# Kernel tuning notes

Measured on AMD Instinct MI355X. Metric: run time of the kernel, lower is better.

## Reference

```python
import jax, jax.numpy as jnp
import numpy as np

N_ATOMS = 100000
N_MOLS = 2500
MAX_NB = 10
HID = 256
ATOM_FDIM = 151
FEAT_DIM = 200
FFN_HID = 1024
N_TASKS = 12
LN_EPS = 1e-5


def setup_inputs() -> dict:
    key = jax.random.key(0)
    ks = jax.random.split(key, 12)
    atoms_per_mol = N_ATOMS // N_MOLS  # 40
    starts = jnp.arange(N_MOLS, dtype=jnp.int32) * atoms_per_mol
    sizes = jnp.full((N_MOLS,), atoms_per_mol, dtype=jnp.int32)
    a_scope = jnp.stack([starts, sizes], axis=1)  # [M, 2]
    d_in = HID + ATOM_FDIM  # 407
    d_ff = 4 * HID          # 1024
    d_mol_in = HID + FEAT_DIM  # 456
    def lin(k, fan_in, shape):
        return jax.random.uniform(k, shape, jnp.float32, -1.0, 1.0) / np.sqrt(fan_in)
    return {
        "atom_output": jax.random.normal(ks[0], (N_ATOMS, HID), jnp.float32),
        "original_f_atoms": jax.random.uniform(ks[1], (N_ATOMS, ATOM_FDIM), jnp.float32),
        "a2a": jax.random.randint(ks[2], (N_ATOMS, MAX_NB), 0, N_ATOMS, jnp.int32),
        "a_scope": a_scope,
        "features_batch": jax.random.normal(ks[3], (N_MOLS, FEAT_DIM), jnp.float32),
        "W1": lin(ks[4], d_in, (d_in, d_ff)), "b1": jnp.zeros((d_ff,), jnp.float32),
        "W2": lin(ks[5], d_ff, (d_ff, HID)), "b2": jnp.zeros((HID,), jnp.float32),
        "ln_g": jnp.ones((HID,), jnp.float32), "ln_b": jnp.zeros((HID,), jnp.float32),
        "Wm1": lin(ks[6], d_mol_in, (d_mol_in, FFN_HID)), "bm1": jnp.zeros((FFN_HID,), jnp.float32),
        "Wm2": lin(ks[7], FFN_HID, (FFN_HID, N_TASKS)), "bm2": jnp.zeros((N_TASKS,), jnp.float32),
    }


def reference(atom_output, original_f_atoms, a2a, a_scope, features_batch,
              W1, b1, W2, b2, ln_g, ln_b, Wm1, bm1, Wm2, bm2):
    # select_neighbor_and_aggregate: gather neighbor embeddings and sum
    aggr = atom_output[a2a].sum(axis=1)                      # [N, HID]
    x = jnp.concatenate([original_f_atoms, aggr], axis=1)    # [N, HID+ATOM_FDIM]
    # PositionwiseFeedForward (dropout = identity at eval)
    h = jax.nn.relu(x @ W1 + b1) @ W2 + b2                   # [N, HID]
    # SublayerConnection with x=None: LayerNorm (dropout identity)
    mu = h.mean(axis=-1, keepdims=True)
    var = ((h - mu) ** 2).mean(axis=-1, keepdims=True)
    h = (h - mu) * jax.lax.rsqrt(var + LN_EPS) * ln_g + ln_b
    # Readout: mean over variable-length a_scope ranges (segment mean)
    starts = a_scope[:, 0]
    sizes = a_scope[:, 1]
    n_mols = a_scope.shape[0]
    seg_ids = jnp.searchsorted(starts, jnp.arange(h.shape[0], dtype=starts.dtype), side="right") - 1
    sums = jax.ops.segment_sum(h, seg_ids, num_segments=n_mols)   # [M, HID]
    mol = sums / sizes[:, None].astype(h.dtype)
    # concat molecule-level features, then mol FFN (2 layers)
    mol = jnp.concatenate([mol, features_batch], axis=1)          # [M, HID+FEAT_DIM]
    out = jax.nn.relu(mol @ Wm1 + bm1) @ Wm2 + bm2                # [M, N_TASKS]
    return out
```

## Files before the change

### kernel.cpp

```cpp
#include <hip/hip_runtime.h>

typedef __attribute__((ext_vector_type(8))) short bfrag;
typedef __attribute__((ext_vector_type(4))) float f32x4;

__device__ __forceinline__ float bf2f(unsigned short u) {
    union { unsigned u32; float f; } cv; cv.u32 = ((unsigned)u) << 16; return cv.f;
}
__device__ __forceinline__ unsigned short f2bf(float f) {
    union { float f; unsigned u; } cv; cv.f = f;
    unsigned u = cv.u;
    unsigned r = (u + 0x7fffu + ((u >> 16) & 1u)) >> 16;
    return (unsigned short)r;
}
__device__ __forceinline__ void gll16(const void* g, void* l) {
    __builtin_amdgcn_global_load_lds(
        (const __attribute__((address_space(1))) unsigned int*)g,
        (__attribute__((address_space(3))) unsigned int*)l, 16, 0, 0);
}

__global__ void to_bf16(const float* __restrict__ src, unsigned short* __restrict__ dst, size_t n) {
    size_t i = ((size_t)blockIdx.x * 256 + threadIdx.x) * 8;
    if (i >= n) return;
    f32x4 a = __builtin_nontemporal_load(reinterpret_cast<const f32x4*>(src + i));
    f32x4 b = __builtin_nontemporal_load(reinterpret_cast<const f32x4*>(src + i + 4));
    ushort4 o0 = {f2bf(a.x), f2bf(a.y), f2bf(a.z), f2bf(a.w)};
    ushort4 o1 = {f2bf(b.x), f2bf(b.y), f2bf(b.z), f2bf(b.w)};
    *reinterpret_cast<ushort4*>(dst + i) = o0;
    *reinterpret_cast<ushort4*>(dst + i + 4) = o1;
}

__global__ void transpose_pad(const float* __restrict__ W, unsigned short* __restrict__ WT,
                              int R, int Cn, int Kp, int split, int shiftA, int split2, int shiftB) {
    __shared__ unsigned short tile[32][33];
    int r0 = blockIdx.x * 32, c0 = blockIdx.y * 32;
#pragma unroll
    for (int j = 0; j < 4; j++) {
        int r = r0 + threadIdx.y + j * 8;
        int c = c0 + threadIdx.x;
        float v = (r < R) ? W[(size_t)r * Cn + c] : 0.f;
        tile[threadIdx.y + j * 8][threadIdx.x] = f2bf(v);
    }
    __syncthreads();
#pragma unroll
    for (int j = 0; j < 4; j++) {
        int c = c0 + threadIdx.y + j * 8;
        int r = r0 + threadIdx.x;
        int kn = (r < split) ? r + shiftA : (r < split2 ? r + shiftB : r);
        WT[(size_t)c * Kp + kn] = tile[threadIdx.x][threadIdx.y + j * 8];
    }
}

__global__ __launch_bounds__(256) void gather2(const unsigned short* __restrict__ abf,
                                               const float* __restrict__ f_atoms,
                                               const int* __restrict__ a2a,
                                               unsigned short* __restrict__ xb, int n_real) {
    int r = blockIdx.x * 4 + (threadIdx.x >> 6);
    int lane = threadIdx.x & 63;
    unsigned short* xrow = xb + (size_t)r * 448;
    if (r >= n_real) {
        *reinterpret_cast<ushort4*>(xrow + lane * 4) = ushort4{0, 0, 0, 0};
        if (lane < 48) *reinterpret_cast<ushort4*>(xrow + 256 + lane * 4) = ushort4{0, 0, 0, 0};
        return;
    }
    int v = (lane < 10) ? a2a[(size_t)r * 10 + lane] : 0;
    ushort4 u[10];
#pragma unroll
    for (int j = 0; j < 10; j++) {
        int nbj = __shfl(v, j);
        u[j] = *reinterpret_cast<const ushort4*>(abf + (size_t)nbj * 256 + lane * 4);
    }
    float a0 = 0.f, a1 = 0.f, a2 = 0.f, a3 = 0.f;
#pragma unroll
    for (int j = 0; j < 10; j++) {
        a0 += bf2f(u[j].x);
        a1 += bf2f(u[j].y);
        a2 += bf2f(u[j].z);
        a3 += bf2f(u[j].w);
    }
    ushort4 o = {f2bf(a0), f2bf(a1), f2bf(a2), f2bf(a3)};
    *reinterpret_cast<ushort4*>(xrow + lane * 4) = o;
    const float* fr = f_atoms + (size_t)r * 151;
#pragma unroll
    for (int s = 0; s < 3; s++) {
        int c = lane + s * 64;
        if (c < 151) xrow[256 + c] = f2bf(__builtin_nontemporal_load(fr + c));
    }
    if (lane < 41) xrow[407 + lane] = 0;
}

template <int RELU>
__global__ __launch_bounds__(512, 2) void gemm256(const unsigned short* __restrict__ A,
                                                  const unsigned short* __restrict__ BT,
                                                  const float* __restrict__ bias,
                                                  unsigned short* __restrict__ C,
                                                  int NB, int N, int K) {
    __shared__ __align__(16) unsigned short As[256 * 64];
    __shared__ __align__(16) unsigned short Bs[128 * 64];
    const int t = threadIdx.x;
    const int lane = t & 63, wid = t >> 6;
    const int wm = wid >> 1, wn = wid & 1;
    const int la = lane & 15, hi = lane >> 4;

    const int nwg = gridDim.x, orig = blockIdx.x;
    const int q = nwg >> 3, r8 = nwg & 7;
    const int xcd = orig & 7, slot = orig >> 3;
    const int wgid = (xcd < r8 ? xcd * (q + 1) : r8 * (q + 1) + (xcd - r8) * q) + slot;
    const int bm = (wgid / NB) * 256, bn = (wgid % NB) * 128;

    f32x4 acc[4][4] = {};

    const int tr = t >> 3, ts = t & 7;
    const unsigned short* Ag = A + (size_t)(bm + tr) * K + (ts ^ (tr & 7)) * 8;
    const unsigned short* Bg = BT + (size_t)(bn + tr) * K + (ts ^ (tr & 7)) * 8;
    const int ldst = tr * 64 + ts * 8;

    for (int kt = 0; kt < K; kt += 64) {
        __builtin_amdgcn_s_barrier();
#pragma unroll
        for (int p = 0; p < 4; p++) gll16(Ag + (size_t)(p * 64) * K + kt, &As[p * 4096 + ldst]);
#pragma unroll
        for (int p = 0; p < 2; p++) gll16(Bg + (size_t)(p * 64) * K + kt, &Bs[p * 4096 + ldst]);
        asm volatile("s_waitcnt vmcnt(0)" ::: "memory");
        __builtin_amdgcn_s_barrier();
#pragma unroll
        for (int kk = 0; kk < 2; kk++) {
            bfrag a[4], b[4];
#pragma unroll
            for (int i = 0; i < 4; i++) {
                int row = wm * 64 + i * 16 + la;
                a[i] = *reinterpret_cast<const bfrag*>(&As[row * 64 + (((kk * 4 + hi) ^ (la & 7)) * 8)]);
            }
#pragma unroll
            for (int j = 0; j < 4; j++) {
                int row = wn * 64 + j * 16 + la;
                b[j] = *reinterpret_cast<const bfrag*>(&Bs[row * 64 + (((kk * 4 + hi) ^ (la & 7)) * 8)]);
            }
#pragma unroll
            for (int i = 0; i < 4; i++)
#pragma unroll
                for (int j = 0; j < 4; j++)
                    acc[i][j] = __builtin_amdgcn_mfma_f32_16x16x32_bf16(a[i], b[j], acc[i][j], 0, 0, 0);
        }
    }

#pragma unroll
    for (int j = 0; j < 4; j++) {
        int col = bn + wn * 64 + j * 16 + la;
        float bv = bias[col];
#pragma unroll
        for (int i = 0; i < 4; i++) {
            int rbase = bm + wm * 64 + i * 16 + hi * 4;
#pragma unroll
            for (int r = 0; r < 4; r++) {
                float v = acc[i][j][r] + bv;
                if (RELU) v = fmaxf(v, 0.f);
                C[(size_t)(rbase + r) * N + col] = f2bf(v);
            }
        }
    }
}

__global__ __launch_bounds__(512, 2) void gemm2k(const unsigned short* __restrict__ A,
                                                 const unsigned short* __restrict__ BT,
                                                 const float* __restrict__ bias,
                                                 unsigned short* __restrict__ C, int K) {
    __shared__ __align__(16) unsigned short As[128 * 64];
    __shared__ __align__(16) unsigned short Bs[256 * 64];
    const int t = threadIdx.x;
    const int lane = t & 63, wid = t >> 6;
    const int wm = wid >> 2, wn = wid & 3;
    const int la = lane & 15, hi = lane >> 4;
    const int N = 256;

    const int nwg = gridDim.x, orig = blockIdx.x;
    const int q = nwg >> 3, r8 = nwg & 7;
    const int xcd = orig & 7, slot = orig >> 3;
    const int wgid = (xcd < r8 ? xcd * (q + 1) : r8 * (q + 1) + (xcd - r8) * q) + slot;
    const int bm = wgid * 128;

    f32x4 acc[4][4] = {};

    const int tr = t >> 3, ts = t & 7;
    const unsigned short* Ag = A + (size_t)(bm + tr) * K + (ts ^ (tr & 7)) * 8;
    const unsigned short* Bg = BT + (size_t)tr * K + (ts ^ (tr & 7)) * 8;
    const int ldst = tr * 64 + ts * 8;

    for (int kt = 0; kt < K; kt += 64) {
        __builtin_amdgcn_s_barrier();
#pragma unroll
        for (int p = 0; p < 2; p++) gll16(Ag + (size_t)(p * 64) * K + kt, &As[p * 4096 + ldst]);
#pragma unroll
        for (int p = 0; p < 4; p++) gll16(Bg + (size_t)(p * 64) * K + kt, &Bs[p * 4096 + ldst]);
        asm volatile("s_waitcnt vmcnt(0)" ::: "memory");
        __builtin_amdgcn_s_barrier();
#pragma unroll
        for (int kk = 0; kk < 2; kk++) {
            bfrag a[4], b[4];
#pragma unroll
            for (int i = 0; i < 4; i++) {
                int row = wm * 64 + i * 16 + la;
                a[i] = *reinterpret_cast<const bfrag*>(&As[row * 64 + (((kk * 4 + hi) ^ (la & 7)) * 8)]);
            }
#pragma unroll
            for (int j = 0; j < 4; j++) {
                int row = wn * 64 + j * 16 + la;
                b[j] = *reinterpret_cast<const bfrag*>(&Bs[row * 64 + (((kk * 4 + hi) ^ (la & 7)) * 8)]);
            }
#pragma unroll
            for (int i = 0; i < 4; i++)
#pragma unroll
                for (int j = 0; j < 4; j++)
                    acc[i][j] = __builtin_amdgcn_mfma_f32_16x16x32_bf16(a[i], b[j], acc[i][j], 0, 0, 0);
        }
    }

#pragma unroll
    for (int j = 0; j < 4; j++) {
        int col = wn * 64 + j * 16 + la;
        float bv = bias[col];
#pragma unroll
        for (int i = 0; i < 4; i++) {
            int rbase = bm + wm * 64 + i * 16 + hi * 4;
#pragma unroll
            for (int r = 0; r < 4; r++)
                C[(size_t)(rbase + r) * N + col] = f2bf(acc[i][j][r] + bv);
        }
    }
}

__global__ __launch_bounds__(512) void seg_ln_mean(const unsigned short* __restrict__ h,
                                                   const int* __restrict__ a_scope,
                                                   const float* __restrict__ g,
                                                   const float* __restrict__ b,
                                                   const float* __restrict__ feats,
                                                   unsigned short* __restrict__ mol, int n_mols) {
    __shared__ float part[8][256];
    int m = blockIdx.x, t = threadIdx.x;
    unsigned short* mrow = mol + (size_t)m * 512;
    if (m >= n_mols) {
        mrow[t] = 0;
        return;
    }
    int w = t >> 6, lane = t & 63;
    int start = a_scope[2 * m], size = a_scope[2 * m + 1];
    float4 gv = *reinterpret_cast<const float4*>(g + lane * 4);
    float4 bv = *reinterpret_cast<const float4*>(b + lane * 4);
    float a0 = 0.f, a1 = 0.f, a2 = 0.f, a3 = 0.f;
    for (int r = w; r < size; r += 8) {
        const unsigned short* hp = h + (size_t)(start + r) * 256 + lane * 4;
        ushort4 u = *reinterpret_cast<const ushort4*>(hp);
        float v0 = bf2f(u.x), v1 = bf2f(u.y), v2 = bf2f(u.z), v3 = bf2f(u.w);
        float s = v0 + v1 + v2 + v3;
        float q2 = v0 * v0 + v1 * v1 + v2 * v2 + v3 * v3;
#pragma unroll
        for (int off = 32; off; off >>= 1) {
            s += __shfl_xor(s, off);
            q2 += __shfl_xor(q2, off);
        }
        float mean = s * (1.f / 256.f);
        float var = q2 * (1.f / 256.f) - mean * mean;
        float rs = rsqrtf(var + 1e-5f);
        a0 += (v0 - mean) * rs * gv.x + bv.x;
        a1 += (v1 - mean) * rs * gv.y + bv.y;
        a2 += (v2 - mean) * rs * gv.z + bv.z;
        a3 += (v3 - mean) * rs * gv.w + bv.w;
    }
    part[w][lane * 4 + 0] = a0;
    part[w][lane * 4 + 1] = a1;
    part[w][lane * 4 + 2] = a2;
    part[w][lane * 4 + 3] = a3;
    __syncthreads();
    if (t < 256) {
        float sum = 0.f;
#pragma unroll
        for (int i = 0; i < 8; i++) sum += part[i][t];
        mrow[t] = f2bf(sum / (float)size);
    } else {
        int c = t - 256;
        float fv = (c < 200) ? feats[(size_t)m * 200 + c] : 0.f;
        mrow[256 + c] = f2bf(fv);
    }
}

__global__ void ffn2(const unsigned short* __restrict__ m1, const float* __restrict__ Wm2,
                     const float* __restrict__ bm2, float* __restrict__ out, int n_mols) {
    int wid = blockIdx.x * 4 + (threadIdx.x >> 6);
    if (wid >= n_mols) return;
    int lane = threadIdx.x & 63;
    float acc[12] = {};
    const unsigned short* row = m1 + (size_t)wid * 1024;
#pragma unroll 4
    for (int i = 0; i < 16; i++) {
        int k = i * 64 + lane;
        float v = bf2f(row[k]);
        const float* wr_ = Wm2 + (size_t)k * 12;
#pragma unroll
        for (int tsk = 0; tsk < 12; tsk++) acc[tsk] += v * wr_[tsk];
    }
#pragma unroll
    for (int tsk = 0; tsk < 12; tsk++) {
        float sv = acc[tsk];
#pragma unroll
        for (int off = 32; off; off >>= 1) sv += __shfl_xor(sv, off);
        if (lane == 0) out[(size_t)wid * 12 + tsk] = sv + bm2[tsk];
    }
}

extern "C" void kernel_launch(void* const* d_in, const int* in_sizes, int n_in,
                              void* d_out, int out_size, void* d_ws, size_t ws_size,
                              hipStream_t stream) {
    const float* atom_output = (const float*)d_in[0];
    const float* f_atoms     = (const float*)d_in[1];
    const int*   a2a         = (const int*)d_in[2];
    const int*   a_scope     = (const int*)d_in[3];
    const float* feats       = (const float*)d_in[4];
    const float* W1  = (const float*)d_in[5];
    const float* b1  = (const float*)d_in[6];
    const float* W2  = (const float*)d_in[7];
    const float* b2  = (const float*)d_in[8];
    const float* ln_g = (const float*)d_in[9];
    const float* ln_b = (const float*)d_in[10];
    const float* Wm1 = (const float*)d_in[11];
    const float* bm1 = (const float*)d_in[12];
    const float* Wm2 = (const float*)d_in[13];
    const float* bm2 = (const float*)d_in[14];
    float* out = (float*)d_out;

    char* ws = (char*)d_ws;
    size_t off = 0;
    auto alloc = [&](size_t bytes) {
        void* p = ws + off;
        off += (bytes + 255) & ~(size_t)255;
        return p;
    };
    unsigned short* h     = (unsigned short*)alloc((size_t)100096 * 256 * 2);
    unsigned short* h1    = (unsigned short*)alloc((size_t)100096 * 1024 * 2);
    unsigned short* xf    = (unsigned short*)alloc((size_t)100096 * 448 * 2);
    unsigned short* mol   = (unsigned short*)alloc((size_t)2560 * 512 * 2);
    unsigned short* m1b   = (unsigned short*)alloc((size_t)2560 * 1024 * 2);
    unsigned short* W1bT  = (unsigned short*)alloc((size_t)1024 * 448 * 2);
    unsigned short* W2bT  = (unsigned short*)alloc((size_t)256 * 1024 * 2);
    unsigned short* Wm1bT = (unsigned short*)alloc((size_t)1024 * 512 * 2);
    unsigned short* abf   = h1;

    transpose_pad<<<dim3(14, 32), dim3(32, 8), 0, stream>>>(W1, W1bT, 407, 1024, 448, 151, 256, 407, -151);
    transpose_pad<<<dim3(32, 8),  dim3(32, 8), 0, stream>>>(W2, W2bT, 1024, 256, 1024, 0, 0, 0, 0);
    transpose_pad<<<dim3(16, 32), dim3(32, 8), 0, stream>>>(Wm1, Wm1bT, 456, 1024, 512, 0, 0, 0, 0);

    to_bf16<<<12500, 256, 0, stream>>>(atom_output, abf, (size_t)100000 * 256);
    gather2<<<25024, 256, 0, stream>>>(abf, f_atoms, a2a, xf, 100000);

    gemm256<1><<<391 * 8, 512, 0, stream>>>(xf, W1bT, b1, h1, 8, 1024, 448);
    gemm2k<<<782, 512, 0, stream>>>(h1, W2bT, b2, h, 1024);

    seg_ln_mean<<<2560, 512, 0, stream>>>(h, a_scope, ln_g, ln_b, feats, mol, 2500);
    gemm256<1><<<10 * 8, 512, 0, stream>>>(mol, Wm1bT, bm1, m1b, 8, 1024, 512);
    ffn2<<<625, 256, 0, stream>>>(m1b, Wm2, bm2, out, 2500);
}
```

Baseline: 391.0 us.

## Add double-buffered K=32 pipelined GEMM for first atom FFN layer

Introduces gemm1p, a 256x128-tile bf16 MFMA GEMM that stages K in 32-wide slices into two LDS buffers via global_load_lds. The next two slices are prefetched while the current one computes, using a vmcnt wait so only the needed loads are awaited. It uses a swizzled LDS layout to avoid bank conflicts. The aim is to hide global load latency in the first FFN layer. The cost is two barriers per 32-wide K step instead of fewer, larger steps, and the epilogue writes scalar bf16 stores.

```diff
diff --git a/kernel.cpp b/kernel.cpp
--- a/kernel.cpp
+++ b/kernel.cpp
@@ -86,6 +86,81 @@
         if (c < 151) xrow[256 + c] = f2bf(__builtin_nontemporal_load(fr + c));
     }
     if (lane < 41) xrow[407 + lane] = 0;
+}
+
+__global__ __launch_bounds__(512, 2) void gemm1p(const unsigned short* __restrict__ A,
+                                                 const unsigned short* __restrict__ BT,
+                                                 const float* __restrict__ bias,
+                                                 unsigned short* __restrict__ C,
+                                                 int NB, int N, int K) {
+    __shared__ __align__(16) unsigned short As[2][256 * 32];
+    __shared__ __align__(16) unsigned short Bs[2][128 * 32];
+    const int t = threadIdx.x;
+    const int lane = t & 63, wid = t >> 6;
+    const int wm = wid >> 1, wn = wid & 1;
+    const int la = lane & 15, hi = lane >> 4;
+
+    const int nwg = gridDim.x, orig = blockIdx.x;
+    const int q = nwg >> 3, r8 = nwg & 7;
+    const int xcd = orig & 7, slot = orig >> 3;
+    const int wgid = (xcd < r8 ? xcd * (q + 1) : r8 * (q + 1) + (xcd - r8) * q) + slot;
+    const int bm = (wgid / NB) * 256, bn = (wgid % NB) * 128;
+
+    f32x4 acc[4][4] = {};
+
+    const int tr = t >> 2, ts = t & 3;
+    const int koff = ((ts - ((tr >> 1) & 3)) & 3) * 8;
+    const unsigned short* Ag = A + (size_t)(bm + tr) * K + koff;
+    const unsigned short* Bg = BT + (size_t)(bn + tr) * K + koff;
+    const int ldst = tr * 32 + ts * 8;
+
+    auto stage = [&](int buf, int kt) {
+        gll16(Ag + kt, &As[buf][ldst]);
+        gll16(Ag + (size_t)128 * K + kt, &As[buf][4096 + ldst]);
+        gll16(Bg + kt, &Bs[buf][ldst]);
+    };
+
+    const int NT = K >> 5;
+    stage(0, 0);
+    stage(1, 32);
+
+    const int slotOff = ((hi + ((la >> 1) & 3)) & 3) * 8;
+    int cur = 0;
+    for (int it = 0; it < NT; ++it) {
+        if (it + 1 < NT) asm volatile("s_waitcnt vmcnt(3)" ::: "memory");
+        else             asm volatile("s_waitcnt vmcnt(0)" ::: "memory");
+        __builtin_amdgcn_s_barrier();
+        bfrag a[4], b[4];
+#pragma unroll
+        for (int i = 0; i < 4; i++)
+            a[i] = *reinterpret_cast<const bfrag*>(&As[cur][(wm * 64 + i * 16 + la) * 32 + slotOff]);
+#pragma unroll
+        for (int j = 0; j < 4; j++)
+            b[j] = *reinterpret_cast<const bfrag*>(&Bs[cur][(wn * 64 + j * 16 + la) * 32 + slotOff]);
+#pragma unroll
+        for (int i = 0; i < 4; i++)
+#pragma unroll
+            for (int j = 0; j < 4; j++)
+                acc[i][j] = __builtin_amdgcn_mfma_f32_16x16x32_bf16(a[i], b[j], acc[i][j], 0, 0, 0);
+        __builtin_amdgcn_s_barrier();
+        if (it + 2 < NT) stage(cur, (it + 2) * 32);
+        cur ^= 1;
+    }
+
+#pragma unroll
+    for (int j = 0; j < 4; j++) {
+        int col = bn + wn * 64 + j * 16 + la;
+        float bv = bias[col];
+#pragma unroll
+        for (int i = 0; i < 4; i++) {
+            int rbase = bm + wm * 64 + i * 16 + hi * 4;
+#pragma unroll
+            for (int r = 0; r < 4; r++) {
+                float v = fmaxf(acc[i][j][r] + bv, 0.f);
+                C[(size_t)(rbase + r) * N + col] = f2bf(v);
+            }
+        }
+    }
 }
 
 template <int RELU>
@@ -350,7 +425,7 @@
     to_bf16<<<12500, 256, 0, stream>>>(atom_output, abf, (size_t)100000 * 256);
     gather2<<<25024, 256, 0, stream>>>(abf, f_atoms, a2a, xf, 100000);
 
-    gemm256<1><<<391 * 8, 512, 0, stream>>>(xf, W1bT, b1, h1, 8, 1024, 448);
+    gemm1p<<<391 * 8, 512, 0, stream>>>(xf, W1bT, b1, h1, 8, 1024, 448);
     gemm2k<<<782, 512, 0, stream>>>(h1, W2bT, b2, h, 1024);
 
     seg_ln_mean<<<2560, 512, 0, stream>>>(h, a_scope, ln_g, ln_b, feats, mol, 2500);
```

Measured after the change: 397.5 us. About the same (+1.7%).
